# Performance work log

Hardware: AMD Instinct MI355X
Metric: run time of the kernel (lower is better)

The kernel has to match this reference:

```python
import jax, jax.numpy as jnp
import numpy as np

B, C, F, J = 64, 16, 2048, 25
EMBED, CLASSES, NJ = 64, 5, 12
AFFECT = slice(0, 12)
UNAFFECT = slice(12, 24)


def setup_inputs() -> dict:
    key = jax.random.key(0)
    k0, k1, k2, k3 = jax.random.split(key, 4)
    features = jax.random.normal(k0, (B, C, F, J), dtype=jnp.float32)
    W1 = jax.random.normal(k1, (EMBED, C, NJ), dtype=jnp.float32) * 0.05
    b1 = jnp.zeros((EMBED,), jnp.float32)
    W2 = jax.random.normal(k2, (EMBED, C, NJ), dtype=jnp.float32) * 0.05
    b2 = jnp.zeros((EMBED,), jnp.float32)
    Wl = jax.random.normal(k3, (CLASSES, 16 * EMBED), dtype=jnp.float32) * 0.02
    bl = jnp.zeros((CLASSES,), jnp.float32)
    return {"features": features, "W1": W1, "b1": b1, "W2": W2, "b2": b2, "Wl": Wl, "bl": bl}


def _stat_features(x, proto):
    # x: [b, c, f, j]; single sort shared by min/max/quantiles/median
    f = x.shape[-2]
    xs = jnp.sort(x, axis=-2)

    def quant(p):
        # torch.quantile linear interpolation
        pos = p * (f - 1)
        lo = int(np.floor(pos)); hi = int(np.ceil(pos)); frac = np.float32(pos - lo)
        return xs[..., lo, :] * (1.0 - frac) + xs[..., hi, :] * frac

    s1 = xs[..., 0, :]                       # min
    s2 = xs[..., -1, :]                      # max
    s3 = quant(0.25)
    s4 = xs[..., (f - 1) // 2, :]            # torch.median: lower middle element
    s5 = quant(0.75)
    s6 = jnp.mean(x, axis=-2)
    s7 = jnp.std(x, axis=-2, ddof=1)         # torch.std unbiased
    s8 = s2 - s1
    z = (x - s6[..., None, :]) / s7[..., None, :]
    if proto:
        s9 = jnp.mean(z ** 3, axis=-2)       # skew
    else:
        s9 = jnp.mean(z ** 4, axis=-2) - 3.0  # excess kurtosis
    return jnp.stack([s2, s3, s4, s5, s6, s7, s8, s9], axis=-2)  # [b, c, 8, j]


def _fuse(stat, W, b):
    # Conv2d kernel (1, joints) == contraction over (c, j) per stat row
    out = jnp.einsum('bcsj,ecj->bes', stat, W) + b[None, :, None]
    return out.reshape(out.shape[0], -1)  # flatten (embed, stats) like torch.flatten


def reference(features, W1, b1, W2, b2, Wl, bl):
    affected = features[:, :, :, AFFECT]
    unaffected = features[:, :, :, UNAFFECT]
    stat_af = _stat_features(affected, proto=False)
    stat_ua = _stat_features(unaffected, proto=False)
    # attn=False path (STAT_VA block disabled)
    stat1 = _stat_features(unaffected + affected, proto=True)
    _ = _fuse(stat1, W1, b1)  # stat1 branch only feeds CL loss (get_cl_loss=False)
    stat2 = jnp.concatenate([stat_af, stat_ua], axis=-2)  # [b, c, 16, j]
    flat2 = _fuse(stat2, W2, b2)                          # [b, 16*embed]
    logits = flat2 @ Wl.T + bl
    return logits
```

## Files before the change

kernel.cpp:

```cpp
#include <hip/hip_runtime.h>
#include <hip/hip_bf16.h>
#include <math.h>


#define F_LEN 2048
#define JTOT 25
#define STATS_PER_BC 192
#define LP 2056

typedef float f4a __attribute__((ext_vector_type(4), aligned(4)));

template <int PAT>
__device__ __forceinline__ float ds_swz(float v) {
  return __int_as_float(
      __builtin_amdgcn_ds_swizzle(__float_as_int(v), PAT));
}

template <int CTRL, int BANK>
__device__ __forceinline__ int upd_dpp(int old_, int src) {
  return __builtin_amdgcn_update_dpp(old_, src, CTRL, 0xF, BANK, false);
}

__device__ __forceinline__ float xpartner(float v, const int lm,
                                          const int addr32) {
  const int vi = __float_as_int(v);
  switch (lm) {
    case 1:
      return __int_as_float(upd_dpp<0xB1, 0xF>(vi, vi));
    case 2:
      return __int_as_float(upd_dpp<0x4E, 0xF>(vi, vi));
    case 4: {
      const int t1 = upd_dpp<0x104, 0x5>(vi, vi);
      const int t2 = upd_dpp<0x114, 0xA>(t1, vi);
      return __int_as_float(t2);
    }
    case 8:
      return __int_as_float(upd_dpp<0x128, 0xF>(vi, vi));
    case 16:
      return ds_swz<0x401F>(v);
    default:
      return __int_as_float(
          __builtin_amdgcn_ds_bpermute(addr32, vi));
  }
}

__device__ __forceinline__ float wave_sum(float v, int addr32) {
  v += xpartner(v, 1, addr32);
  v += xpartner(v, 2, addr32);
  v += xpartner(v, 4, addr32);
  v += xpartner(v, 8, addr32);
  v += xpartner(v, 16, addr32);
  v += xpartner(v, 32, addr32);
  return v;
}

__device__ __forceinline__ void read_x(const float* wlds, int lane,
                                       float* x) {
  const float4* src4 = (const float4*)wlds;
#pragma unroll
  for (int q = 0; q < 8; ++q) {
    float4 v = src4[lane * 8 + ((lane + q) & 7)];
    x[4 * q] = v.x;
    x[4 * q + 1] = v.y;
    x[4 * q + 2] = v.z;
    x[4 * q + 3] = v.w;
  }
}

__global__ __launch_bounds__(256) void stat_kernel(
    const float* __restrict__ Fp, float* __restrict__ stat2) {
  __shared__ float lds[2 * LP];
  const int g = blockIdx.x;
  const int xcd = g & 7;
  const int mm = g >> 3;
  const int bc = xcd * 128 + mm / 6;
  const int grp = mm % 6;
  const int t = threadIdx.x;
  const int w = t >> 6;
  const int lane = t & 63;
  const int addr32 = ((lane ^ 32) << 2);
  const int j0 = grp * 4;

  float vz[8], vw[8];
  const int rot = (t + ((t >> 5) << 2)) & 31;
  float* p0 = lds + (t & ~31) + rot;
  {
    const float* bbase = Fp + (size_t)bc * F_LEN * JTOT + j0;
#pragma unroll
    for (int it = 0; it < 8; ++it) {
      const int f = it * 256 + t;
      f4a v = *reinterpret_cast<const f4a*>(bbase + (size_t)f * JTOT);
      p0[it * 256] = v.x;
      p0[LP + it * 256] = v.y;
      vz[it] = v.z;
      vw[it] = v.w;
    }
  }
  __syncthreads();

  float x[32];
  if (w < 2) read_x(lds + w * LP, lane, x);
  __syncthreads();

  {
#pragma unroll
    for (int it = 0; it < 8; ++it) {
      p0[it * 256] = vz[it];
      p0[LP + it * 256] = vw[it];
    }
  }
  __syncthreads();
  if (w >= 2) read_x(lds + (w - 2) * LP, lane, x);

  float sum = 0.f;
#pragma unroll
  for (int e = 0; e < 32; ++e) sum += x[e];
  sum = wave_sum(sum, addr32);
  const float m = sum * (1.0f / 2048.0f);

  float c2 = 0.f, c4 = 0.f;
#pragma unroll
  for (int e = 0; e < 32; ++e) {
    float d = x[e] - m;
    float dd = d * d;
    c2 += dd;
    c4 += dd * dd;
  }
  c2 = wave_sum(c2, addr32);
  c4 = wave_sum(c4, addr32);
  const float var = c2 * (1.0f / 2047.0f);
  const float sd = sqrtf(var);
  const float kurt = (c4 * (1.0f / 2048.0f)) / (var * var) - 3.0f;

#pragma unroll
  for (int kp = 1; kp <= 4; ++kp) {
    const int k = 1 << kp;
#pragma unroll
    for (int jp = kp - 1; jp >= 0; --jp) {
      const int st = 1 << jp;
#pragma unroll
      for (int e = 0; e < 32; ++e) {
        if ((e & st) == 0) {
          const bool up = ((e & k) == 0);
          float a = x[e], b = x[e + st];
          float lo2 = fminf(a, b), hi2 = fmaxf(a, b);
          x[e] = up ? lo2 : hi2;
          x[e + st] = up ? hi2 : lo2;
        }
      }
    }
  }

  unsigned Fst = 0u;
#pragma unroll
  for (int kp = 5; kp <= 11; ++kp) {
    const unsigned d = ((lane >> (kp - 5)) & 1) ? 0x80000000u : 0u;
#pragma unroll
    for (int jp = kp - 1; jp >= 5; --jp) {
      const int lm = 1 << (jp - 5);
      const unsigned r = ((lane >> (jp - 5)) & 1) ? 0x80000000u : 0u;
      const unsigned tgt = d ^ r;
      const unsigned fl = tgt ^ Fst;
      Fst = tgt;
#pragma unroll
      for (int e = 0; e < 32; ++e)
        x[e] = __uint_as_float(__float_as_uint(x[e]) ^ fl);
#pragma unroll
      for (int e = 0; e < 32; ++e) {
        float o = xpartner(x[e], lm, addr32);
        x[e] = fminf(x[e], -o);
      }
    }
    {
      const unsigned fl = d ^ Fst;
      Fst = d;
#pragma unroll
      for (int e = 0; e < 32; ++e)
        x[e] = __uint_as_float(__float_as_uint(x[e]) ^ fl);
    }
#pragma unroll
    for (int jp = 4; jp >= 0; --jp) {
      const int st = 1 << jp;
#pragma unroll
      for (int e = 0; e < 32; ++e) {
        if ((e & st) == 0) {
          float a = x[e], b = x[e + st];
          x[e] = fminf(a, b);
          x[e + st] = fmaxf(a, b);
        }
      }
    }
  }

  const float mn = __shfl(x[0], 0, 64);
  const float a511 = __shfl(x[31], 15, 64);
  const float a512 = __shfl(x[0], 16, 64);
  const float amed = __shfl(x[31], 31, 64);
  const float a1535 = __shfl(x[31], 47, 64);
  const float a1536 = __shfl(x[0], 48, 64);
  const float mx = __shfl(x[31], 63, 64);

  if (lane == 0) {
    const float q25 = 0.25f * a511 + 0.75f * a512;
    const float q75 = 0.75f * a1535 + 0.25f * a1536;
    const int j = j0 + w;
    const int jj = (j < 12) ? j : j - 12;
    const int sb = (j < 12) ? 0 : 8;
    float st8[8] = {mx, q25, amed, q75, m, sd, mx - mn, kurt};
    float* o = stat2 + (bc * 16 + sb) * 12 + jj;
#pragma unroll
    for (int s2 = 0; s2 < 8; ++s2) o[s2 * 12] = st8[s2];
  }
}

__global__ __launch_bounds__(256) void prep_kernel(
    const float* __restrict__ W2, const float* __restrict__ b2,
    const float* __restrict__ Wl, const float* __restrict__ bl,
    float* __restrict__ M, float* __restrict__ C) {
  const int g = blockIdx.x;
  const int t = threadIdx.x;
  if (g < 60) {
    const int id = g * 256 + t;
    const int k = id / 3072;
    const int r = id % 3072;
    const int c = r / 192;
    const int s = (r % 192) / 12;
    const int j = r % 12;
    const float* wl = Wl + k * 1024 + s;
    const float* w2 = W2 + c * 12 + j;
    float acc = 0.f;
#pragma unroll 8
    for (int e = 0; e < 64; ++e) acc += wl[e * 16] * w2[e * 192];
    M[id] = acc;
  } else if (t < 64) {
    const int e = t;
    const int addr32 = ((e ^ 32) << 2);
    for (int k = 0; k < 5; ++k) {
      const float* wl = Wl + k * 1024 + e * 16;
      float rs = 0.f;
#pragma unroll
      for (int s = 0; s < 16; ++s) rs += wl[s];
      float v = wave_sum(rs * b2[e], addr32);
      if (e == 0) C[k] = v + bl[k];
    }
  }
}

__global__ __launch_bounds__(256) void logits_kernel(
    const float* __restrict__ stat2, const float* __restrict__ M,
    const float* __restrict__ C, float* __restrict__ out) {
  __shared__ float s_red[20];
  const int b = blockIdx.x;
  const int t = threadIdx.x;
  const int lane = t & 63;
  const int w = t >> 6;
  const int addr32 = ((lane ^ 32) << 2);

  float acc[5] = {0.f, 0.f, 0.f, 0.f, 0.f};
#pragma unroll
  for (int ii = 0; ii < 12; ++ii) {
    const int i = ii * 256 + t;
    const float s = stat2[b * 3072 + i];
#pragma unroll
    for (int k = 0; k < 5; ++k) acc[k] += s * M[k * 3072 + i];
  }
#pragma unroll
  for (int k = 0; k < 5; ++k) acc[k] = wave_sum(acc[k], addr32);
  if (lane == 0) {
#pragma unroll
    for (int k = 0; k < 5; ++k) s_red[w * 5 + k] = acc[k];
  }
  __syncthreads();
  if (t < 5)
    out[b * 5 + t] =
        s_red[t] + s_red[5 + t] + s_red[10 + t] + s_red[15 + t] + C[t];
}

extern "C" void kernel_launch(void* const* d_in, const int* in_sizes, int n_in,
                              void* d_out, int out_size, void* d_ws,
                              size_t ws_size, hipStream_t stream) {
  const float* Fp = (const float*)d_in[0];
  const float* W2 = (const float*)d_in[3];
  const float* b2 = (const float*)d_in[4];
  const float* Wl = (const float*)d_in[5];
  const float* bl = (const float*)d_in[6];
  float* out = (float*)d_out;

  float* stat2 = (float*)d_ws;
  float* M = stat2 + 196608;
  float* C = M + 15360;

  prep_kernel<<<61, 256, 0, stream>>>(W2, b2, Wl, bl, M, C);
  stat_kernel<<<6144, 256, 0, stream>>>(Fp, stat2);
  logits_kernel<<<64, 256, 0, stream>>>(stat2, M, C, out);
}
```

Baseline: 461.7 us.

## Replace final bitonic merge stage with LDS merge-path selection of order statistics

Stops the bitonic sort one stage early, leaving two sorted halves of 1024 elements each. The halves are written to LDS, and five lanes each run a binary-search merge-path to pull out the 511/512/1023/1535/1536th order statistics, with min and max taken from the ends of the halves. This removes the most expensive cross-lane sort stage, at the cost of extra LDS writes, barriers and serial LDS lookups by only a few lanes. The change also splits the partner-exchange loop so all swizzles issue before the min operations, and adds an occupancy hint to the launch bounds.

```diff
diff --git a/kernel.cpp b/kernel.cpp
--- a/kernel.cpp
+++ b/kernel.cpp
@@ -9,6 +9,10 @@
 #define LP 2056
 
 typedef float f4a __attribute__((ext_vector_type(4), aligned(4)));
+
+__device__ __forceinline__ int swz(int i) {
+  return (i & ~31) | ((i + ((i >> 5) << 2)) & 31);
+}
 
 template <int PAT>
 __device__ __forceinline__ float ds_swz(float v) {
@@ -67,7 +71,46 @@
   }
 }
 
-__global__ __launch_bounds__(256) void stat_kernel(
+__device__ __forceinline__ void merge7(const float* wlds, int lane,
+                                       float& val, float& mn, float& mx) {
+  const int kk = (lane == 0) ? 511
+               : (lane == 1) ? 512
+               : (lane == 2) ? 1023
+               : (lane == 3) ? 1535 : 1536;
+  const int mtot = kk + 1;
+  int lo = mtot - 1024; if (lo < 0) lo = 0;
+  int hi = (mtot < 1024) ? mtot : 1024;
+  for (int it = 0; it < 11; ++it) {
+    const bool act = lo < hi;
+    const int s = (lo + hi) >> 1;
+    const int sa = (s < 1023) ? s : 1023;
+    float Av = wlds[swz(sa)];
+    Av = (s < 1024) ? Av : INFINITY;
+    int bidx = mtot - s - 1;
+    bidx = bidx < 0 ? 0 : (bidx > 1023 ? 1023 : bidx);
+    const float Bv = wlds[swz(2047 - bidx)];
+    const bool gg = act && (Bv > Av);
+    if (gg) lo = s + 1;
+    else if (act) hi = s;
+  }
+  {
+    const int s = lo;
+    const int ia = (s - 1 < 0) ? 0 : s - 1;
+    const float fa = wlds[swz(ia)];
+    const float fromA = (s > 0) ? fa : -INFINITY;
+    const int bi = mtot - s - 1;
+    const int ib = (bi < 0) ? 0 : bi;
+    const float fb = wlds[swz(2047 - ib)];
+    const float fromB = (bi >= 0) ? fb : -INFINITY;
+    val = fmaxf(fromA, fromB);
+  }
+  if (lane == 0) {
+    mn = fminf(wlds[swz(0)], wlds[swz(2047)]);
+    mx = fmaxf(wlds[swz(1023)], wlds[swz(1024)]);
+  }
+}
+
+__global__ __launch_bounds__(256, 4) void stat_kernel(
     const float* __restrict__ Fp, float* __restrict__ stat2) {
   __shared__ float lds[2 * LP];
   const int g = blockIdx.x;
@@ -153,7 +196,7 @@
 
   unsigned Fst = 0u;
 #pragma unroll
-  for (int kp = 5; kp <= 11; ++kp) {
+  for (int kp = 5; kp <= 10; ++kp) {
     const unsigned d = ((lane >> (kp - 5)) & 1) ? 0x80000000u : 0u;
 #pragma unroll
     for (int jp = kp - 1; jp >= 5; --jp) {
@@ -162,14 +205,15 @@
       const unsigned tgt = d ^ r;
       const unsigned fl = tgt ^ Fst;
       Fst = tgt;
+      float o[32];
 #pragma unroll
       for (int e = 0; e < 32; ++e)
         x[e] = __uint_as_float(__float_as_uint(x[e]) ^ fl);
 #pragma unroll
-      for (int e = 0; e < 32; ++e) {
-        float o = xpartner(x[e], lm, addr32);
-        x[e] = fminf(x[e], -o);
-      }
+      for (int e = 0; e < 32; ++e) o[e] = xpartner(x[e], lm, addr32);
+#pragma unroll
+      for (int e = 0; e < 32; ++e)
+        x[e] = fminf(x[e], -o[e]);
     }
     {
       const unsigned fl = d ^ Fst;
@@ -191,14 +235,39 @@
       }
     }
   }
-
-  const float mn = __shfl(x[0], 0, 64);
-  const float a511 = __shfl(x[31], 15, 64);
-  const float a512 = __shfl(x[0], 16, 64);
-  const float amed = __shfl(x[31], 31, 64);
-  const float a1535 = __shfl(x[31], 47, 64);
-  const float a1536 = __shfl(x[0], 48, 64);
-  const float mx = __shfl(x[31], 63, 64);
+#pragma unroll
+  for (int e = 0; e < 32; ++e)
+    x[e] = __uint_as_float(__float_as_uint(x[e]) ^ Fst);
+
+  float* wl2 = lds + (w & 1) * LP;
+  float val = 0.f, mn = 0.f, mx = 0.f;
+  if (w < 2) {
+    float4* dst4 = (float4*)wl2;
+#pragma unroll
+    for (int q = 0; q < 8; ++q) {
+      int wq = 8 * lane + ((q + lane) & 7);
+      dst4[wq] = make_float4(x[4 * q], x[4 * q + 1], x[4 * q + 2], x[4 * q + 3]);
+    }
+  }
+  __syncthreads();
+  if (w < 2) merge7(wl2, lane, val, mn, mx);
+  __syncthreads();
+  if (w >= 2) {
+    float4* dst4 = (float4*)wl2;
+#pragma unroll
+    for (int q = 0; q < 8; ++q) {
+      int wq = 8 * lane + ((q + lane) & 7);
+      dst4[wq] = make_float4(x[4 * q], x[4 * q + 1], x[4 * q + 2], x[4 * q + 3]);
+    }
+  }
+  __syncthreads();
+  if (w >= 2) merge7(wl2, lane, val, mn, mx);
+
+  const float a511 = __shfl(val, 0, 64);
+  const float a512 = __shfl(val, 1, 64);
+  const float amed = __shfl(val, 2, 64);
+  const float a1535 = __shfl(val, 3, 64);
+  const float a1536 = __shfl(val, 4, 64);
 
   if (lane == 0) {
     const float q25 = 0.25f * a511 + 0.75f * a512;
```

Result: faster. 449.3 us (-2.7%).
